# Performance work log

Hardware: AMD Instinct MI355X
Metric: run time of the kernel (lower is better)

## Reference

```python
import jax, jax.numpy as jnp
import numpy as np

N_NODES = 100_000
N_EDGES = 1_600_000
IN_CH = 128
HIDDEN = 48
OUT_CH = 16
NEG_SLOPE = 0.2  # PyG GATConv default LeakyReLU slope


def setup_inputs() -> dict:
    key = jax.random.key(0)
    ks = jax.random.split(key, 8)
    x = jax.random.normal(ks[0], (N_NODES, IN_CH), dtype=jnp.float32)
    edge_index = jax.random.randint(ks[1], (2, N_EDGES), 0, N_NODES, dtype=jnp.int64)
    W = jax.random.normal(ks[2], (IN_CH, HIDDEN), dtype=jnp.float32) / np.sqrt(IN_CH)
    att_src = jax.random.normal(ks[3], (HIDDEN,), dtype=jnp.float32) / np.sqrt(HIDDEN)
    att_dst = jax.random.normal(ks[4], (HIDDEN,), dtype=jnp.float32) / np.sqrt(HIDDEN)
    gat_bias = jax.random.normal(ks[5], (HIDDEN,), dtype=jnp.float32) * 0.01
    lin_W = jax.random.normal(ks[6], (HIDDEN, OUT_CH), dtype=jnp.float32) / np.sqrt(HIDDEN)
    lin_b = jax.random.normal(ks[7], (OUT_CH,), dtype=jnp.float32) * 0.01
    return {"x": x, "edge_index": edge_index, "W": W, "att_src": att_src,
            "att_dst": att_dst, "gat_bias": gat_bias, "lin_W": lin_W, "lin_b": lin_b}


def reference(x, edge_index, W, att_src, att_dst, gat_bias, lin_W, lin_b):
    n = x.shape[0]
    # PyG GATConv adds self loops by default
    loops = jnp.arange(n, dtype=edge_index.dtype)
    src = jnp.concatenate([edge_index[0], loops])  # [E+N] message sources j
    dst = jnp.concatenate([edge_index[1], loops])  # [E+N] message targets i

    h = x @ W                      # [N, H] transformed node features
    a_src = h @ att_src            # [N] per-node source attention term
    a_dst = h @ att_dst            # [N] per-node destination attention term

    logits = jax.nn.leaky_relu(a_src[src] + a_dst[dst], NEG_SLOPE)  # [E+N]
    # segment softmax over incoming edges of each destination node
    m = jax.ops.segment_max(logits, dst, num_segments=n)            # [N]
    e = jnp.exp(logits - m[dst])
    denom = jax.ops.segment_sum(e, dst, num_segments=n)             # [N] (>0: self loop)
    alpha = e / denom[dst]                                          # [E+N]

    agg = jax.ops.segment_sum(h[src] * alpha[:, None], dst, num_segments=n)
    out = jax.nn.elu(agg + gat_bias)          # [N, H]
    # dropout is identity in eval mode
    z = out @ lin_W + lin_b                   # [N, OUT]
    return jax.nn.log_softmax(z, axis=-1)
```

## Files before the change

kernel.cpp:

```cpp
#include <hip/hip_runtime.h>
#include <hip/hip_fp16.h>

#define IN_CH 128
#define HID 48
#define OUT_CH 16
#define NEG_SLOPE 0.2f
#define SCAN_ELEMS 2048
#define ROWB 128

__device__ __forceinline__ float leaky(float x) { return x >= 0.f ? x : NEG_SLOPE * x; }
__device__ __forceinline__ float elu(float x) { return x > 0.f ? x : __expf(x) - 1.f; }

__device__ __forceinline__ void load_edge(const void* ei, int E, int is64, int e,
                                          int& s, int& d) {
    if (is64) {
        const long long* p = (const long long*)ei;
        s = (int)p[e];
        d = (int)p[(size_t)E + e];
    } else {
        const int* p = (const int*)ei;
        s = p[e];
        d = p[(size_t)E + e];
    }
}

__global__ void k_detect(const unsigned* __restrict__ ei, int* __restrict__ flag) {
    if (threadIdx.x == 0 && blockIdx.x == 0) {
        unsigned s = 0;
        for (int i = 1; i < 128; i += 2) s |= ei[i];
        *flag = (s == 0) ? 1 : 0;
    }
}

#define BLK_NODES 256
__global__ __launch_bounds__(256, 2) void k_xw(const float* __restrict__ x,
                                               const float* __restrict__ W,
                                               const float* __restrict__ att_src,
                                               const float* __restrict__ att_dst,
                                               __half* __restrict__ h2,
                                               float* __restrict__ a_src,
                                               float* __restrict__ a_dst,
                                               int* __restrict__ deg, int N) {
    __shared__ float Wl[IN_CH * HID];
    __shared__ float xl[BLK_NODES * 33];
    const int t = threadIdx.x;
    for (int i = t; i < IN_CH * HID / 4; i += 256)
        ((float4*)Wl)[i] = ((const float4*)W)[i];
    const int n0 = blockIdx.x * BLK_NODES;
    const int kq = t & 3;
    const int ng = t >> 2;
    const int k0 = kq * 12;

    float acc[4][12];
#pragma unroll
    for (int i = 0; i < 4; ++i)
#pragma unroll
        for (int j = 0; j < 12; ++j) acc[i][j] = 0.f;

    for (int c0 = 0; c0 < IN_CH; c0 += 32) {
        __syncthreads();
#pragma unroll
        for (int p = 0; p < 8; ++p) {
            int id = t + p * 256;
            int row = id >> 3;
            int seg = id & 7;
            int n = n0 + row;
            float4 v = make_float4(0.f, 0.f, 0.f, 0.f);
            if (n < N) v = ((const float4*)(x + (size_t)n * IN_CH + c0))[seg];
            float* dst = &xl[row * 33 + seg * 4];
            dst[0] = v.x; dst[1] = v.y; dst[2] = v.z; dst[3] = v.w;
        }
        __syncthreads();
#pragma unroll 8
        for (int cc = 0; cc < 32; ++cc) {
            int c = c0 + cc;
            float xv[4];
#pragma unroll
            for (int i = 0; i < 4; ++i) xv[i] = xl[(ng * 4 + i) * 33 + cc];
            const float* wr = &Wl[c * HID + k0];
#pragma unroll
            for (int j = 0; j < 12; ++j) {
                float wv = wr[j];
#pragma unroll
                for (int i = 0; i < 4; ++i) acc[i][j] += xv[i] * wv;
            }
        }
    }
#pragma unroll
    for (int i = 0; i < 4; ++i) {
        int n = n0 + ng * 4 + i;
        if (n < N) {
            uint* dst = (uint*)((char*)h2 + (size_t)n * ROWB) + k0 / 2;
#pragma unroll
            for (int j = 0; j < 6; ++j) {
                __half2 hv = __floats2half2_rn(acc[i][2 * j], acc[i][2 * j + 1]);
                dst[j] = *(const uint*)&hv;
            }
        }
    }
#pragma unroll
    for (int p = 0; p < 8; ++p) {
        int id = t + p * 256;
        int row = id >> 3;
        int seg = id & 7;
        int n = n0 + row;
        if (n < N) ((uint*)((char*)h2 + (size_t)n * ROWB))[24 + seg] = 0u;
    }
    float as_[4], ad_[4];
#pragma unroll
    for (int i = 0; i < 4; ++i) {
        float s1 = 0.f, s2 = 0.f;
#pragma unroll
        for (int j = 0; j < 12; ++j) {
            float a = acc[i][j];
            s1 += a * att_src[k0 + j];
            s2 += a * att_dst[k0 + j];
        }
        s1 += __shfl_xor(s1, 1); s1 += __shfl_xor(s1, 2);
        s2 += __shfl_xor(s2, 1); s2 += __shfl_xor(s2, 2);
        as_[i] = s1; ad_[i] = s2;
    }
    if (kq == 0) {
#pragma unroll
        for (int i = 0; i < 4; ++i) {
            int n = n0 + ng * 4 + i;
            if (n < N) { a_src[n] = as_[i]; a_dst[n] = ad_[i]; }
        }
    }
    {
        int n = n0 + t;
        if (n < N) deg[n] = 0;
    }
}

__global__ __launch_bounds__(256) void k_count(const void* __restrict__ ei,
                                               const int* __restrict__ flag,
                                               int* __restrict__ deg,
                                               int* __restrict__ rank, int E) {
    int e = blockIdx.x * blockDim.x + threadIdx.x;
    if (e >= E) return;
    int d = (*flag) ? (int)((const long long*)ei)[(size_t)E + e]
                    : ((const int*)ei)[(size_t)E + e];
    rank[e] = atomicAdd(&deg[d], 1);
}

__global__ __launch_bounds__(256) void k_scan_block(const int* __restrict__ deg,
                                                    int* __restrict__ rowptr,
                                                    int* __restrict__ bsum, int N) {
    __shared__ int sm[256];
    const int t = threadIdx.x;
    const int base = blockIdx.x * SCAN_ELEMS + t * 8;
    int v[8];
    int s = 0;
#pragma unroll
    for (int i = 0; i < 8; ++i) {
        v[i] = (base + i < N) ? deg[base + i] : 0;
        s += v[i];
    }
    sm[t] = s;
    __syncthreads();
    for (int off = 1; off < 256; off <<= 1) {
        int y = (t >= off) ? sm[t - off] : 0;
        __syncthreads();
        sm[t] += y;
        __syncthreads();
    }
    int run = sm[t] - s;
#pragma unroll
    for (int i = 0; i < 8; ++i) {
        if (base + i < N) rowptr[base + i] = run;
        run += v[i];
    }
    if (t == 255) bsum[blockIdx.x] = sm[255];
}

__global__ __launch_bounds__(256) void k_scan_add(int* __restrict__ rowptr,
                                                  const int* __restrict__ bsum, int N, int E) {
    __shared__ int soff;
    const int chunk = (int)(((long long)blockIdx.x * 256) / SCAN_ELEMS);
    if (threadIdx.x == 0) {
        int run = 0;
        for (int b = 0; b < chunk; ++b) run += bsum[b];
        soff = run;
    }
    __syncthreads();
    int i = blockIdx.x * 256 + threadIdx.x;
    if (i == 0) rowptr[N] = E;
    if (i >= N) return;
    rowptr[i] += soff;
}

__global__ __launch_bounds__(256) void k_scatter(const void* __restrict__ ei,
                                                 const int* __restrict__ flag,
                                                 const float* __restrict__ a_src,
                                                 const float* __restrict__ a_dst,
                                                 const int* __restrict__ rowptr,
                                                 const int* __restrict__ rank,
                                                 unsigned long long* __restrict__ packed,
                                                 int E) {
    int e = blockIdx.x * blockDim.x + threadIdx.x;
    if (e >= E) return;
    int is64 = *flag;
    int s, d;
    load_edge(ei, E, is64, e, s, d);
    int pos = rowptr[d] + rank[e];
    float l = leaky(a_src[s] + a_dst[d]);
    float ev = __expf(fminf(l, 50.f));
    unsigned long long u = ((unsigned long long)__float_as_uint(ev) << 32) | (unsigned)s;
    __builtin_nontemporal_store(u, packed + pos);
}

__global__ __launch_bounds__(256) void k_gat_node(const int* __restrict__ rowptr,
                                                  const unsigned long long* __restrict__ packed,
                                                  const float* __restrict__ a_src,
                                                  const float* __restrict__ a_dst,
                                                  const __half* __restrict__ h2,
                                                  const float* __restrict__ gat_bias,
                                                  const float* __restrict__ lin_W,
                                                  const float* __restrict__ lin_b,
                                                  float* __restrict__ out, int N) {
    __shared__ float Wl[HID * OUT_CH];
    __shared__ float lb[OUT_CH];
    __shared__ float gb[HID];
    __shared__ float o_sm[4][HID];
    const int t = threadIdx.x;
    for (int i = t; i < HID * OUT_CH; i += 256) Wl[i] = lin_W[i];
    if (t < OUT_CH) lb[t] = lin_b[t];
    if (t >= 64 && t < 64 + HID) gb[t - 64] = gat_bias[t - 64];
    __syncthreads();

    const int wv = t >> 6;
    const int lane = t & 63;
    const int slot = lane >> 4;
    const int c = lane & 15;
    const int n = blockIdx.x * 4 + wv;
    const bool active = n < N;

    if (active) {
        const int base = rowptr[n];
        const int deg = rowptr[n + 1] - base;
        const float self_l = leaky(a_src[n] + a_dst[n]);
        const float ev_self = __expf(fminf(self_l, 50.f));
        const char* hb = (const char*)h2;

        float a0 = 0.f, a1 = 0.f, a2 = 0.f, a3 = 0.f, evsum = 0.f;
        if (slot == 0) {
            evsum = ev_self;
            uint2 hv = *(const uint2*)(hb + (size_t)n * ROWB + 8 * c);
            float2 f0 = __half22float2(*(const __half2*)&hv.x);
            float2 f1 = __half22float2(*(const __half2*)&hv.y);
            a0 = ev_self * f0.x; a1 = ev_self * f0.y;
            a2 = ev_self * f1.x; a3 = ev_self * f1.y;
        }
        int j = slot;
#pragma unroll 2
        for (; j + 4 < deg; j += 8) {
            unsigned long long pr0 = packed[base + j];
            unsigned long long pr1 = packed[base + j + 4];
            uint2 hv0 = *(const uint2*)(hb + (size_t)(unsigned)pr0 * ROWB + 8 * c);
            uint2 hv1 = *(const uint2*)(hb + (size_t)(unsigned)pr1 * ROWB + 8 * c);
            float ev0 = __uint_as_float((unsigned)(pr0 >> 32));
            float ev1 = __uint_as_float((unsigned)(pr1 >> 32));
            float2 f00 = __half22float2(*(const __half2*)&hv0.x);
            float2 f01 = __half22float2(*(const __half2*)&hv0.y);
            float2 f10 = __half22float2(*(const __half2*)&hv1.x);
            float2 f11 = __half22float2(*(const __half2*)&hv1.y);
            evsum += ev0; evsum += ev1;
            a0 += ev0 * f00.x; a1 += ev0 * f00.y;
            a2 += ev0 * f01.x; a3 += ev0 * f01.y;
            a0 += ev1 * f10.x; a1 += ev1 * f10.y;
            a2 += ev1 * f11.x; a3 += ev1 * f11.y;
        }
        if (j < deg) {
            unsigned long long pr = packed[base + j];
            float ev = __uint_as_float((unsigned)(pr >> 32));
            uint2 hv = *(const uint2*)(hb + (size_t)(unsigned)pr * ROWB + 8 * c);
            float2 f0 = __half22float2(*(const __half2*)&hv.x);
            float2 f1 = __half22float2(*(const __half2*)&hv.y);
            evsum += ev;
            a0 += ev * f0.x; a1 += ev * f0.y;
            a2 += ev * f1.x; a3 += ev * f1.y;
        }
        evsum += __shfl_xor(evsum, 16); evsum += __shfl_xor(evsum, 32);
        a0 += __shfl_xor(a0, 16); a0 += __shfl_xor(a0, 32);
        a1 += __shfl_xor(a1, 16); a1 += __shfl_xor(a1, 32);
        a2 += __shfl_xor(a2, 16); a2 += __shfl_xor(a2, 32);
        a3 += __shfl_xor(a3, 16); a3 += __shfl_xor(a3, 32);
        const float inv = 1.f / evsum;
        if (slot == 0 && c < 12) {
            float4 v = make_float4(elu(a0 * inv + gb[4 * c + 0]),
                                   elu(a1 * inv + gb[4 * c + 1]),
                                   elu(a2 * inv + gb[4 * c + 2]),
                                   elu(a3 * inv + gb[4 * c + 3]));
            *(float4*)&o_sm[wv][4 * c] = v;
        }
    }
    __syncthreads();

    if (active && lane < OUT_CH) {
        float z = lb[lane];
        const float* o = o_sm[wv];
#pragma unroll
        for (int k = 0; k < HID; ++k) z += o[k] * Wl[k * OUT_CH + lane];
        float mx = z;
#pragma unroll
        for (int off = 8; off; off >>= 1) mx = fmaxf(mx, __shfl_xor(mx, off, 16));
        float ev = __expf(z - mx);
#pragma unroll
        for (int off = 8; off; off >>= 1) ev += __shfl_xor(ev, off, 16);
        float lse = mx + __logf(ev);
        out[(size_t)n * OUT_CH + lane] = z - lse;
    }
}

extern "C" void kernel_launch(void* const* d_in, const int* in_sizes, int n_in,
                              void* d_out, int out_size, void* d_ws, size_t ws_size,
                              hipStream_t stream) {
    const float* x = (const float*)d_in[0];
    const void* edge_index = d_in[1];
    const float* W = (const float*)d_in[2];
    const float* att_src = (const float*)d_in[3];
    const float* att_dst = (const float*)d_in[4];
    const float* gat_bias = (const float*)d_in[5];
    const float* lin_W = (const float*)d_in[6];
    const float* lin_b = (const float*)d_in[7];
    float* out = (float*)d_out;

    const int N = in_sizes[0] / IN_CH;
    const int E = in_sizes[1] / 2;

    __half* h2 = (__half*)d_ws;
    float* a_src = (float*)((char*)d_ws + (size_t)N * ROWB);
    float* a_dst = a_src + N;
    int* rank = (int*)(a_dst + N);
    int* rowptr = rank + E;
    int* degbuf = rowptr + N + 1;
    int* bsum = degbuf + N;
    int* flag = bsum + 64;
    unsigned long long* packed =
        (unsigned long long*)(((uintptr_t)(flag + 1) + 7) & ~(uintptr_t)7);

    const int nodeBlocks = (N + 255) / 256;
    const int edgeBlocks = (E + 255) / 256;
    const int scanBlocks = (N + SCAN_ELEMS - 1) / SCAN_ELEMS;

    k_detect<<<1, 64, 0, stream>>>((const unsigned*)edge_index, flag);
    k_xw<<<(N + BLK_NODES - 1) / BLK_NODES, 256, 0, stream>>>(x, W, att_src, att_dst,
                                                              h2, a_src, a_dst, degbuf, N);
    k_count<<<edgeBlocks, 256, 0, stream>>>(edge_index, flag, degbuf, rank, E);
    k_scan_block<<<scanBlocks, 256, 0, stream>>>(degbuf, rowptr, bsum, N);
    k_scan_add<<<nodeBlocks, 256, 0, stream>>>(rowptr, bsum, N, E);
    k_scatter<<<edgeBlocks, 256, 0, stream>>>(edge_index, flag, a_src, a_dst, rowptr,
                                              rank, packed, E);
    k_gat_node<<<(N + 3) / 4, 256, 0, stream>>>(rowptr, packed, a_src, a_dst,
                                                h2, gat_bias, lin_W, lin_b, out, N);
}
```

Baseline: 242.7 us.

## Move edge attention exp into node kernel, shrink rank and CSR buffers

The scatter kernel now writes only 4-byte source indices instead of packed 8-byte (exp, src) pairs, and no longer gathers a_src/a_dst. The node kernel recomputes the attention weight per edge from a gathered a_src plus a cached a_dst. Rank is stored as 16-bit, which halves that buffer but assumes in-degree stays below 65536. The final linear layer is split across all 64 lanes with a padded shared-memory layout and shuffle reduction. The trade is an extra random a_src gather and exp per edge in the node kernel in exchange for less write and read traffic.

New measurement: 236.2 us. 2.7% less time.

```diff
diff --git a/kernel.cpp b/kernel.cpp
--- a/kernel.cpp
+++ b/kernel.cpp
@@ -136,12 +136,12 @@
 __global__ __launch_bounds__(256) void k_count(const void* __restrict__ ei,
                                                const int* __restrict__ flag,
                                                int* __restrict__ deg,
-                                               int* __restrict__ rank, int E) {
+                                               unsigned short* __restrict__ rank, int E) {
     int e = blockIdx.x * blockDim.x + threadIdx.x;
     if (e >= E) return;
     int d = (*flag) ? (int)((const long long*)ei)[(size_t)E + e]
                     : ((const int*)ei)[(size_t)E + e];
-    rank[e] = atomicAdd(&deg[d], 1);
+    rank[e] = (unsigned short)atomicAdd(&deg[d], 1);
 }
 
 __global__ __launch_bounds__(256) void k_scan_block(const int* __restrict__ deg,
@@ -192,26 +192,20 @@
 
 __global__ __launch_bounds__(256) void k_scatter(const void* __restrict__ ei,
                                                  const int* __restrict__ flag,
-                                                 const float* __restrict__ a_src,
-                                                 const float* __restrict__ a_dst,
                                                  const int* __restrict__ rowptr,
-                                                 const int* __restrict__ rank,
-                                                 unsigned long long* __restrict__ packed,
-                                                 int E) {
+                                                 const unsigned short* __restrict__ rank,
+                                                 unsigned* __restrict__ srcs, int E) {
     int e = blockIdx.x * blockDim.x + threadIdx.x;
     if (e >= E) return;
     int is64 = *flag;
     int s, d;
     load_edge(ei, E, is64, e, s, d);
-    int pos = rowptr[d] + rank[e];
-    float l = leaky(a_src[s] + a_dst[d]);
-    float ev = __expf(fminf(l, 50.f));
-    unsigned long long u = ((unsigned long long)__float_as_uint(ev) << 32) | (unsigned)s;
-    __builtin_nontemporal_store(u, packed + pos);
+    int pos = rowptr[d] + (int)rank[e];
+    __builtin_nontemporal_store((unsigned)s, srcs + pos);
 }
 
 __global__ __launch_bounds__(256) void k_gat_node(const int* __restrict__ rowptr,
-                                                  const unsigned long long* __restrict__ packed,
+                                                  const unsigned* __restrict__ srcs,
                                                   const float* __restrict__ a_src,
                                                   const float* __restrict__ a_dst,
                                                   const __half* __restrict__ h2,
@@ -219,12 +213,12 @@
                                                   const float* __restrict__ lin_W,
                                                   const float* __restrict__ lin_b,
                                                   float* __restrict__ out, int N) {
-    __shared__ float Wl[HID * OUT_CH];
+    __shared__ float Wl[HID * 17];
     __shared__ float lb[OUT_CH];
     __shared__ float gb[HID];
     __shared__ float o_sm[4][HID];
     const int t = threadIdx.x;
-    for (int i = t; i < HID * OUT_CH; i += 256) Wl[i] = lin_W[i];
+    for (int i = t; i < HID * OUT_CH; i += 256) Wl[(i >> 4) * 17 + (i & 15)] = lin_W[i];
     if (t < OUT_CH) lb[t] = lin_b[t];
     if (t >= 64 && t < 64 + HID) gb[t - 64] = gat_bias[t - 64];
     __syncthreads();
@@ -239,8 +233,8 @@
     if (active) {
         const int base = rowptr[n];
         const int deg = rowptr[n + 1] - base;
-        const float self_l = leaky(a_src[n] + a_dst[n]);
-        const float ev_self = __expf(fminf(self_l, 50.f));
+        const float adn = a_dst[n];
+        const float ev_self = __expf(fminf(leaky(a_src[n] + adn), 50.f));
         const char* hb = (const char*)h2;
 
         float a0 = 0.f, a1 = 0.f, a2 = 0.f, a3 = 0.f, evsum = 0.f;
@@ -255,12 +249,14 @@
         int j = slot;
 #pragma unroll 2
         for (; j + 4 < deg; j += 8) {
-            unsigned long long pr0 = packed[base + j];
-            unsigned long long pr1 = packed[base + j + 4];
-            uint2 hv0 = *(const uint2*)(hb + (size_t)(unsigned)pr0 * ROWB + 8 * c);
-            uint2 hv1 = *(const uint2*)(hb + (size_t)(unsigned)pr1 * ROWB + 8 * c);
-            float ev0 = __uint_as_float((unsigned)(pr0 >> 32));
-            float ev1 = __uint_as_float((unsigned)(pr1 >> 32));
+            unsigned s0 = srcs[base + j];
+            unsigned s1 = srcs[base + j + 4];
+            float as0 = a_src[s0];
+            float as1 = a_src[s1];
+            uint2 hv0 = *(const uint2*)(hb + (size_t)s0 * ROWB + 8 * c);
+            uint2 hv1 = *(const uint2*)(hb + (size_t)s1 * ROWB + 8 * c);
+            float ev0 = __expf(fminf(leaky(as0 + adn), 50.f));
+            float ev1 = __expf(fminf(leaky(as1 + adn), 50.f));
             float2 f00 = __half22float2(*(const __half2*)&hv0.x);
             float2 f01 = __half22float2(*(const __half2*)&hv0.y);
             float2 f10 = __half22float2(*(const __half2*)&hv1.x);
@@ -272,9 +268,10 @@
             a2 += ev1 * f11.x; a3 += ev1 * f11.y;
         }
         if (j < deg) {
-            unsigned long long pr = packed[base + j];
-            float ev = __uint_as_float((unsigned)(pr >> 32));
-            uint2 hv = *(const uint2*)(hb + (size_t)(unsigned)pr * ROWB + 8 * c);
+            unsigned s0 = srcs[base + j];
+            float as0 = a_src[s0];
+            uint2 hv = *(const uint2*)(hb + (size_t)s0 * ROWB + 8 * c);
+            float ev = __expf(fminf(leaky(as0 + adn), 50.f));
             float2 f0 = __half22float2(*(const __half2*)&hv.x);
             float2 f1 = __half22float2(*(const __half2*)&hv.y);
             evsum += ev;
@@ -297,11 +294,16 @@
     }
     __syncthreads();
 
-    if (active && lane < OUT_CH) {
-        float z = lb[lane];
+    if (active) {
         const float* o = o_sm[wv];
-#pragma unroll
-        for (int k = 0; k < HID; ++k) z += o[k] * Wl[k * OUT_CH + lane];
+        float z = 0.f;
+#pragma unroll
+        for (int i = 0; i < 12; ++i) {
+            int k = 12 * slot + i;
+            z += o[k] * Wl[k * 17 + c];
+        }
+        z += __shfl_xor(z, 16); z += __shfl_xor(z, 32);
+        z += lb[c];
         float mx = z;
 #pragma unroll
         for (int off = 8; off; off >>= 1) mx = fmaxf(mx, __shfl_xor(mx, off, 16));
@@ -309,7 +311,7 @@
 #pragma unroll
         for (int off = 8; off; off >>= 1) ev += __shfl_xor(ev, off, 16);
         float lse = mx + __logf(ev);
-        out[(size_t)n * OUT_CH + lane] = z - lse;
+        if (slot == 0) out[(size_t)n * OUT_CH + c] = z - lse;
     }
 }
 
@@ -332,13 +334,13 @@
     __half* h2 = (__half*)d_ws;
     float* a_src = (float*)((char*)d_ws + (size_t)N * ROWB);
     float* a_dst = a_src + N;
-    int* rank = (int*)(a_dst + N);
-    int* rowptr = rank + E;
+    int* rowptr = (int*)(a_dst + N);
     int* degbuf = rowptr + N + 1;
     int* bsum = degbuf + N;
     int* flag = bsum + 64;
-    unsigned long long* packed =
-        (unsigned long long*)(((uintptr_t)(flag + 1) + 7) & ~(uintptr_t)7);
+    unsigned short* rank = (unsigned short*)(flag + 1);
+    unsigned* srcs =
+        (unsigned*)(((uintptr_t)(rank + E) + 3) & ~(uintptr_t)3);
 
     const int nodeBlocks = (N + 255) / 256;
     const int edgeBlocks = (E + 255) / 256;
@@ -350,8 +352,7 @@
     k_count<<<edgeBlocks, 256, 0, stream>>>(edge_index, flag, degbuf, rank, E);
     k_scan_block<<<scanBlocks, 256, 0, stream>>>(degbuf, rowptr, bsum, N);
     k_scan_add<<<nodeBlocks, 256, 0, stream>>>(rowptr, bsum, N, E);
-    k_scatter<<<edgeBlocks, 256, 0, stream>>>(edge_index, flag, a_src, a_dst, rowptr,
-                                              rank, packed, E);
-    k_gat_node<<<(N + 3) / 4, 256, 0, stream>>>(rowptr, packed, a_src, a_dst,
+    k_scatter<<<edgeBlocks, 256, 0, stream>>>(edge_index, flag, rowptr, rank, srcs, E);
+    k_gat_node<<<(N + 3) / 4, 256, 0, stream>>>(rowptr, srcs, a_src, a_dst,
                                                 h2, gat_bias, lin_W, lin_b, out, N);
 }
```
